# Performance work log

Hardware: AMD Instinct MI355X
Metric: run time of the kernel (lower is better)

The kernel has to match this reference:

```python
import jax, jax.numpy as jnp
import numpy as np

N = 96            # max_nodes == R (all nodes real)
IN_DIM, HID, ZD = 64, 256, 64
E = 1024
U = N * (N - 1) // 2
NUM_LOGITS = U + N   # 4656
MPM_ITERS = 50
BN_EPS = 1e-5

def _xavier_relu(k, fi, fo):
    # xavier_uniform with gain('relu') = sqrt(2)
    s = (2.0 ** 0.5) * (6.0 / (fi + fo)) ** 0.5
    return jax.random.uniform(k, (fi, fo), jnp.float32, -s, s)

def setup_inputs() -> dict:
    key = jax.random.key(0)
    ks = jax.random.split(key, 12)
    x = jax.random.normal(ks[0], (N, IN_DIM), jnp.float32)
    edge_index = jnp.stack([jax.random.randint(ks[1], (E,), 0, N),
                            jax.random.randint(ks[2], (E,), 0, N)]).astype(jnp.int32)
    a = (jax.random.uniform(ks[3], (N, N)) < 0.06).astype(jnp.float32)
    adj_gt = jnp.maximum(a, a.T) * (1.0 - jnp.eye(N, dtype=jnp.float32))
    return dict(
        x=x, edge_index=edge_index, adj_gt=adj_gt,
        W1=_xavier_relu(ks[4], IN_DIM, HID), b1=jnp.zeros(HID, jnp.float32),
        gamma1=jnp.ones(HID, jnp.float32), beta1=jnp.zeros(HID, jnp.float32),
        W2=_xavier_relu(ks[5], HID, HID), b2=jnp.zeros(HID, jnp.float32),
        gamma2=jnp.ones(HID, jnp.float32), beta2=jnp.zeros(HID, jnp.float32),
        Wmu=_xavier_relu(ks[6], HID, ZD), bmu=jnp.zeros(ZD, jnp.float32),
        Wlv=_xavier_relu(ks[7], HID, ZD), blv=jnp.zeros(ZD, jnp.float32),
        Wd1=_xavier_relu(ks[8], ZD, HID), bd1=jnp.zeros(HID, jnp.float32),
        Wd2=_xavier_relu(ks[9], HID, NUM_LOGITS), bd2=jnp.zeros(NUM_LOGITS, jnp.float32),
        eps=jax.random.normal(ks[10], (ZD,), jnp.float32))

def _bn(h, g, b):
    # BatchNorm1d, training mode: normalize over nodes (axis 0)
    m = h.mean(0)
    v = h.var(0)
    return (h - m) * jax.lax.rsqrt(v + BN_EPS) * g + b

def _forward(x, adj_gt, W1, b1, gamma1, beta1, W2, b2, gamma2, beta2,
             Wmu, bmu, Wlv, blv, Wd1, bd1, Wd2, bd2, eps, edge_index):
    ar = jnp.arange(N)
    eye = jnp.eye(N, dtype=bool)
    A = jnp.zeros((N, N), jnp.float32).at[edge_index[0], edge_index[1]].set(1.0)
    A = jnp.maximum(A, jnp.eye(N, dtype=jnp.float32))  # self loops
    dinv = jax.lax.rsqrt(A.sum(1))
    A_norm = A * dinv[:, None] * dinv[None, :]
    h = jax.nn.relu(_bn(A_norm @ (x @ W1) + b1, gamma1, beta1))
    h = jax.nn.relu(_bn(A_norm @ (h @ W2) + b2, gamma2, beta2))
    # ---- readout, reparam, decode ----
    g_vec = h.sum(0) / N                      # divide by real node count R
    mu = g_vec @ Wmu + bmu
    lv = jnp.clip(g_vec @ Wlv + blv, -4.0, 4.0)
    z = mu + eps * jnp.exp(0.5 * lv)
    vec = jnp.tanh(jax.nn.relu(z @ Wd1 + bd1) @ Wd2 + bd2)  # [NUM_LOGITS]
    # ---- vec_to_adj ----
    iu = jnp.triu_indices(N, 1)
    Ah = jnp.zeros((N, N), jnp.float32).at[iu].set(vec[:U])
    Ah = (Ah + Ah.T).at[ar, ar].set(vec[U:])  # adjacency logits
    # ---- edge similarity tensor S[i,j,a,b] ----
    Agt = adj_gt.at[ar, ar].set(1.0)
    B = jax.nn.sigmoid(Ah).at[ar, ar].set(1.0)
    degA, degB = Agt.sum(1), B.sum(1)
    node_sim = 1.0 / (jnp.abs(degA[:, None] - degB[None, :]) + 1.0)  # [N,N]
    dA, dB = jnp.diag(Agt), jnp.diag(B)
    S = (Agt[:, :, None, None] * dA[:, None, None, None] * dA[None, :, None, None]
         * B[None, None, :, :] * dB[None, None, :, None] * dB[None, None, None, :])
    xor = eye[:, :, None, None] ^ eye[None, None, :, :]
    S = jnp.where(xor, 0.0, S)
    diag_val = dA[:, None] * dB[None, :] * node_sim  # value at (i,i,a,a)
    both = eye[:, :, None, None] & eye[None, None, :, :]
    S = jnp.where(both, diag_val[:, None, :, None], S)
    # ---- MPM iteration (fixed 50 steps) ----
    nd = S[ar[:, None], ar[:, None], ar[None, :], ar[None, :]]  # node sim [N,N]
    offmask = (~eye)[:, :, None].astype(S.dtype)                # [N,N,1] over (i,j)
    def step(X, _):
        node_term = X * nd
        XS_max = (S * X[None, :, None, :]).max(-1)  # (i,j,a): max_b X[j,b]*S[i,j,a,b]
        edge_term = (XS_max * offmask).sum(1)       # sum over j != i
        Xn = node_term + edge_term
        Xn = Xn / jnp.linalg.norm(Xn)               # Frobenius norm
        return Xn, None
    X0 = jnp.full((N, N), 1.0 / N, jnp.float32)
    X, _ = jax.lax.scan(jax.checkpoint(step), X0, None, length=MPM_ITERS)
    return X

def reference(x, edge_index, adj_gt, W1, b1, gamma1, beta1, W2, b2, gamma2, beta2,
              Wmu, bmu, Wlv, blv, Wd1, bd1, Wd2, bd2, eps):
    return _forward(x, adj_gt, W1, b1, gamma1, beta1, W2, b2, gamma2, beta2,
                    Wmu, bmu, Wlv, blv, Wd1, bd1, Wd2, bd2, eps, edge_index)
```

## Files before the change

### kernel.cpp

```cpp
#include <hip/hip_runtime.h>
#include <math.h>

#define NN    96
#define EE    1024
#define HID   256
#define IND   64
#define ZD    64
#define NL    4656
#define NBLK  96
#define NTHR  384
#define ITERS 50
#define NBARS 57
#define SHF   (HID*49)

struct Params {
  const float* x; const int* ei; const float* adj;
  const float* W1; const float* b1; const float* g1; const float* be1;
  const float* W2; const float* b2; const float* g2; const float* be2;
  const float* Wmu; const float* bmu; const float* Wlv; const float* blv;
  const float* Wd1; const float* bd1; const float* Wd2; const float* bd2;
  const float* eps; float* out;
};

__device__ float d_XW[NN*HID];
__device__ float d_H1pre[NN*HID];
__device__ float d_HW2[NN*HID];
__device__ float d_H2pre[NN*HID];
__device__ float d_mean1[HID], d_istd1[HID];
__device__ float d_gvec[HID];
__device__ float d_vec[NL];
__device__ float d_Xg[2][NN*NN];
__device__ float d_part[2][NN];
__device__ int   d_flag[NBLK];
__device__ int   d_rel;
__device__ int   d_epoch;

__device__ __forceinline__ float gld(const float* p) {
  return __hip_atomic_load(p, __ATOMIC_RELAXED, __HIP_MEMORY_SCOPE_AGENT);
}
__device__ __forceinline__ void gst(float* p, float v) {
  __hip_atomic_store(p, v, __ATOMIC_RELAXED, __HIP_MEMORY_SCOPE_AGENT);
}

__device__ __forceinline__ float wsum(float v) {
  v += __shfl_xor(v, 32, 64);
  v += __shfl_xor(v, 16, 64);
  v += __shfl_xor(v,  8, 64);
  v += __shfl_xor(v,  4, 64);
  v += __shfl_xor(v,  2, 64);
  v += __shfl_xor(v,  1, 64);
  return v;
}

__device__ __forceinline__ int tri_idx(int a, int c) {
  return a*95 - (a*(a-1))/2 + (c - a - 1);
}

__device__ __forceinline__ void gbar(int idx, int base) {
  asm volatile("s_waitcnt vmcnt(0)" ::: "memory");
  __syncthreads();
  const int tgt = base + idx + 1;
  const int t = threadIdx.x;
  if (blockIdx.x == 0) {
    if (t >= 1 && t < NBLK) {
      while (__hip_atomic_load(&d_flag[t], __ATOMIC_RELAXED, __HIP_MEMORY_SCOPE_AGENT) < tgt)
        __builtin_amdgcn_s_sleep(1);
    }
    __syncthreads();
    if (t == 0)
      __hip_atomic_store(&d_rel, tgt, __ATOMIC_RELAXED, __HIP_MEMORY_SCOPE_AGENT);
  } else {
    if (t == 0) {
      __hip_atomic_store(&d_flag[blockIdx.x], tgt, __ATOMIC_RELAXED, __HIP_MEMORY_SCOPE_AGENT);
      while (__hip_atomic_load(&d_rel, __ATOMIC_RELAXED, __HIP_MEMORY_SCOPE_AGENT) < tgt)
        __builtin_amdgcn_s_sleep(1);
    }
    __syncthreads();
  }
}

__global__ void __launch_bounds__(NTHR) gvae_kernel(Params p) {
  const int b = blockIdx.x;
  const int t = threadIdx.x;

  __shared__ __align__(16) float SH[SHF];
  __shared__ float pre1[HID];
  __shared__ float sg[HID], sd1[HID], sz[ZD];
  __shared__ float dinv[NN];
  __shared__ float eV[NN];   __shared__ int eL[NN];  __shared__ int s_ecnt;
  __shared__ float ndrow[NN], rowsq[NN], xb2[NN];
  __shared__ int   nbrL[NN];
  __shared__ float sdegA;    __shared__ int s_cnt;
  __shared__ float sF;

  const int base = __hip_atomic_load(&d_epoch, __ATOMIC_RELAXED, __HIP_MEMORY_SCOPE_AGENT) * NBARS;

  for (int i = t; i < NN*97; i += NTHR) SH[i] = 0.0f;
  __syncthreads();
  for (int e = t; e < EE; e += NTHR) {
    int s = p.ei[e], d = p.ei[EE + e];
    SH[s*97 + d] = 1.0f;
  }
  if (t < NN) SH[t*97 + t] = 1.0f;
  __syncthreads();
  if (t < NN) {
    float s = 0.0f;
    for (int j = 0; j < NN; ++j) s += SH[t*97 + j];
    dinv[t] = 1.0f / sqrtf(s);
  }
  if (t < 64) {
    bool is1 = SH[b*97 + t] > 0.5f;
    unsigned long long m1 = __ballot(is1);
    if (is1) eL[__popcll(m1 & ((1ull << t) - 1))] = t;
    int c1 = __popcll(m1);
    bool is2 = (t < 32) && SH[b*97 + 64 + t] > 0.5f;
    unsigned long long m2 = __ballot(is2);
    if (is2) eL[c1 + __popcll(m2 & ((1ull << t) - 1))] = 64 + t;
    if (t == 0) s_ecnt = c1 + __popcll(m2);
  }
  __syncthreads();
  if (t < s_ecnt) eV[t] = dinv[b] * dinv[eL[t]];
  if (t < HID) {
    float acc = 0.0f;
    for (int d = 0; d < IND; ++d) acc += p.x[b*IND + d] * p.W1[d*HID + t];
    gst(&d_XW[b*HID + t], acc);
  }
  if (t < NN) gst(&d_Xg[0][b*NN + t], 1.0f/96.0f);
  gbar(0, base);

  {
    const int lim = s_ecnt * HID;
    float tv[16];
    #pragma unroll
    for (int r = 0; r < 16; ++r) {
      int idx = t + r*NTHR;
      if (idx < lim) tv[r] = gld(&d_XW[eL[idx >> 8]*HID + (idx & 255)]);
    }
    #pragma unroll
    for (int r = 0; r < 16; ++r) {
      int idx = t + r*NTHR;
      if (idx < lim) SH[idx] = tv[r];
    }
    for (int idx = t + 16*NTHR; idx < lim; idx += NTHR)
      SH[idx] = gld(&d_XW[eL[idx >> 8]*HID + (idx & 255)]);
    __syncthreads();
    if (t < HID) {
      float acc = 0.0f;
      const int ec = s_ecnt;
      for (int n = 0; n < ec; ++n) acc += eV[n] * SH[n*HID + t];
      acc += p.b1[t];
      pre1[t] = acc;
      gst(&d_H1pre[b*HID + t], acc);
    }
  }
  gbar(1, base);

  if (b < 86) {
    int w = t >> 6, lane = t & 63;
    int c = b*3 + w;
    if (w < 3 && c < HID) {
      float v0 = gld(&d_H1pre[lane*HID + c]);
      float v1 = (lane < 32) ? gld(&d_H1pre[(64+lane)*HID + c]) : 0.0f;
      float mean = wsum(v0 + v1) * (1.0f/96.0f);
      float a0 = v0 - mean, a1 = (lane < 32) ? (v1 - mean) : 0.0f;
      float var = wsum(a0*a0 + a1*a1) * (1.0f/96.0f);
      if (lane == 0) { gst(&d_mean1[c], mean); gst(&d_istd1[c], 1.0f/sqrtf(var + 1e-5f)); }
    }
  }
  gbar(2, base);

  if (t < HID) {
    float m = gld(&d_mean1[t]), is = gld(&d_istd1[t]);
    pre1[t] = fmaxf((pre1[t] - m) * is * p.g1[t] + p.be1[t], 0.0f);
  }
  __syncthreads();
  if (t < HID) {
    float acc = 0.0f;
    for (int k = 0; k < HID; ++k) acc += pre1[k] * p.W2[k*HID + t];
    gst(&d_HW2[b*HID + t], acc);
  }
  gbar(3, base);

  {
    const int lim = s_ecnt * HID;
    float tv[16];
    #pragma unroll
    for (int r = 0; r < 16; ++r) {
      int idx = t + r*NTHR;
      if (idx < lim) tv[r] = gld(&d_HW2[eL[idx >> 8]*HID + (idx & 255)]);
    }
    #pragma unroll
    for (int r = 0; r < 16; ++r) {
      int idx = t + r*NTHR;
      if (idx < lim) SH[idx] = tv[r];
    }
    for (int idx = t + 16*NTHR; idx < lim; idx += NTHR)
      SH[idx] = gld(&d_HW2[eL[idx >> 8]*HID + (idx & 255)]);
    __syncthreads();
    if (t < HID) {
      float acc = 0.0f;
      const int ec = s_ecnt;
      for (int n = 0; n < ec; ++n) acc += eV[n] * SH[n*HID + t];
      acc += p.b2[t];
      gst(&d_H2pre[b*HID + t], acc);
    }
  }
  gbar(4, base);

  if (b < 86) {
    int w = t >> 6, lane = t & 63;
    int c = b*3 + w;
    if (w < 3 && c < HID) {
      float v0 = gld(&d_H2pre[lane*HID + c]);
      float v1 = (lane < 32) ? gld(&d_H2pre[(64+lane)*HID + c]) : 0.0f;
      float mean = wsum(v0 + v1) * (1.0f/96.0f);
      float a0 = v0 - mean, a1 = (lane < 32) ? (v1 - mean) : 0.0f;
      float var = wsum(a0*a0 + a1*a1) * (1.0f/96.0f);
      float is = 1.0f / sqrtf(var + 1e-5f);
      float ga = p.g2[c], be = p.be2[c];
      float h0 = fmaxf((v0 - mean)*is*ga + be, 0.0f);
      float h1v = (lane < 32) ? fmaxf((v1 - mean)*is*ga + be, 0.0f) : 0.0f;
      float gs = wsum(h0 + h1v);
      if (lane == 0) gst(&d_gvec[c], gs * (1.0f/96.0f));
    }
  }
  gbar(5, base);

  if (t < HID) sg[t] = gld(&d_gvec[t]);
  __syncthreads();
  if (t < ZD) {
    float am = p.bmu[t], al = p.blv[t];
    for (int c = 0; c < HID; ++c) {
      float gv = sg[c];
      am += gv * p.Wmu[c*ZD + t];
      al += gv * p.Wlv[c*ZD + t];
    }
    al = fminf(fmaxf(al, -4.0f), 4.0f);
    sz[t] = am + p.eps[t] * expf(0.5f * al);
  }
  __syncthreads();
  if (t < HID) {
    float acc = p.bd1[t];
    for (int d = 0; d < ZD; ++d) acc += sz[d] * p.Wd1[d*HID + t];
    sd1[t] = fmaxf(acc, 0.0f);
  }
  __syncthreads();
  {
    const int o0 = b*49;
    const int nout = min(49, NL - o0);
    #pragma unroll 4
    for (int idx = t; idx < HID*49; idx += NTHR) {
      int k = idx / 49, o = idx - k*49;
      SH[idx] = (o0 + o < NL) ? p.Wd2[k*NL + o0 + o] : 0.0f;
    }
    __syncthreads();
    if (t < nout) {
      float acc = p.bd2[o0 + t];
      for (int k = 0; k < HID; ++k) acc += sd1[k] * SH[k*49 + t];
      gst(&d_vec[o0 + t], tanhf(acc));
    }
  }
  gbar(6, base);

  {
    float tv[13];
    #pragma unroll
    for (int r = 0; r < 13; ++r) {
      int idx = t + r*NTHR;
      if (idx < NL) tv[r] = gld(&d_vec[idx]);
    }
    #pragma unroll
    for (int r = 0; r < 13; ++r) {
      int idx = t + r*NTHR;
      if (idx < NL) SH[idx] = tv[r];
    }
  }
  const int kk = t >> 2;
  const int qq = t & 3;
  if (t < 64) {
    float s = p.adj[b*NN + t] + ((t < 32) ? p.adj[b*NN + 64 + t] : 0.0f);
    s = wsum(s);
    if (t == 0) sdegA = s + 1.0f;
    bool is1 = (t != b) && (p.adj[b*NN + t] > 0.5f);
    unsigned long long m1 = __ballot(is1);
    if (is1) nbrL[__popcll(m1 & ((1ull << t) - 1))] = t;
    int c1 = __popcll(m1);
    bool is2 = (t < 32) && ((64 + t) != b) && (p.adj[b*NN + 64 + t] > 0.5f);
    unsigned long long m2 = __ballot(is2);
    if (is2) nbrL[c1 + __popcll(m2 & ((1ull << t) - 1))] = 64 + t;
    if (t == 0) s_cnt = c1 + __popcll(m2);
  }
  __syncthreads();

  float breg[24];
  {
    float bs = 0.0f;
    const int lb = qq*24;
    #pragma unroll
    for (int s = 0; s < 24; ++s) {
      int l = lb + s;
      float v = 0.0f;
      if (l != kk) {
        int a  = kk < l ? kk : l;
        int cc = kk < l ? l : kk;
        v = 1.0f / (1.0f + expf(-SH[tri_idx(a, cc)]));
      }
      breg[s] = v;
      bs += v;
    }
    float tot = bs + __shfl_xor(bs, 1, 64);
    tot += __shfl_xor(tot, 2, 64);
    if (qq == 0) ndrow[kk] = 1.0f / (fabsf(sdegA - (tot + 1.0f)) + 1.0f);
  }
  __syncthreads();

  int cur = 0;
  for (int it = 0; it < ITERS; ++it) {
    const int cnt = s_cnt;
    const int lim = (cnt + 1) * NN;
    const float* Xs = d_Xg[cur];
    float pj = 0.0f;
    if (it > 0 && t < NN) pj = gld(&d_part[(it-1) & 1][t]);
    float tv[8];
    #pragma unroll
    for (int r = 0; r < 8; ++r) {
      int idx = t + r*NTHR;
      if (idx < lim) {
        int slot = idx / NN, col = idx - slot*NN;
        int j = (slot == cnt) ? b : nbrL[slot];
        tv[r] = gld(&Xs[j*NN + col]);
      }
    }
    float s2 = 1.0f;
    if (it > 0) {
      if (t < NN) rowsq[t] = pj;
      __syncthreads();
      if (t < 64) {
        float v = rowsq[t] + ((t < 32) ? rowsq[64 + t] : 0.0f);
        v = wsum(v);
        if (t == 0) sF = v;
      }
      __syncthreads();
      s2 = sF;
    }
    int ex;
    (void)frexpf(sqrtf(s2), &ex);
    const float scale = ldexpf(1.0f, -ex);
    #pragma unroll
    for (int r = 0; r < 8; ++r) {
      int idx = t + r*NTHR;
      if (idx < lim) SH[idx] = tv[r];
    }
    for (int idx = t + 8*NTHR; idx < lim; idx += NTHR) {
      int slot = idx / NN, col = idx - slot*NN;
      int j = (slot == cnt) ? b : nbrL[slot];
      SH[idx] = gld(&Xs[j*NN + col]);
    }
    __syncthreads();

    float acc = 0.0f;
    for (int n = 0; n < cnt; ++n) {
      const float4* xp = reinterpret_cast<const float4*>(&SH[n*NN + qq*24]);
      float vm = 0.0f;
      #pragma unroll
      for (int s6 = 0; s6 < 6; ++s6) {
        float4 xv = xp[s6];
        vm = fmaxf(vm, breg[4*s6+0] * xv.x);
        vm = fmaxf(vm, breg[4*s6+1] * xv.y);
        vm = fmaxf(vm, breg[4*s6+2] * xv.z);
        vm = fmaxf(vm, breg[4*s6+3] * xv.w);
      }
      vm = fmaxf(vm, __shfl_xor(vm, 1, 64));
      vm = fmaxf(vm, __shfl_xor(vm, 2, 64));
      acc += vm;
    }
    if (qq == 0) {
      float xn = scale * (SH[cnt*NN + kk] * ndrow[kk] + acc);
      xb2[kk] = xn;
      rowsq[kk] = xn * xn;
      gst(&d_Xg[cur ^ 1][b*NN + kk], xn);
    }
    __syncthreads();
    if (t < 64) {
      float v = rowsq[t] + ((t < 32) ? rowsq[64 + t] : 0.0f);
      v = wsum(v);
      if (t == 0) gst(&d_part[it & 1][b], v);
    }
    gbar(7 + it, base);
    cur ^= 1;
  }

  if (t < NN) rowsq[t] = gld(&d_part[(ITERS-1) & 1][t]);
  __syncthreads();
  if (t < 64) {
    float v = rowsq[t] + ((t < 32) ? rowsq[64 + t] : 0.0f);
    v = wsum(v);
    if (t == 0) sF = v;
  }
  __syncthreads();
  if (t < NN) p.out[b*NN + t] = xb2[t] * (1.0f / sqrtf(sF));

  if (b == 0 && t == 0)
    __hip_atomic_fetch_add(&d_epoch, 1, __ATOMIC_RELAXED, __HIP_MEMORY_SCOPE_AGENT);
}

extern "C" void kernel_launch(void* const* d_in, const int* in_sizes, int n_in,
                              void* d_out, int out_size, void* d_ws, size_t ws_size,
                              hipStream_t stream) {
  Params prm;
  prm.x   = (const float*)d_in[0];
  prm.ei  = (const int*  )d_in[1];
  prm.adj = (const float*)d_in[2];
  prm.W1  = (const float*)d_in[3];
  prm.b1  = (const float*)d_in[4];
  prm.g1  = (const float*)d_in[5];
  prm.be1 = (const float*)d_in[6];
  prm.W2  = (const float*)d_in[7];
  prm.b2  = (const float*)d_in[8];
  prm.g2  = (const float*)d_in[9];
  prm.be2 = (const float*)d_in[10];
  prm.Wmu = (const float*)d_in[11];
  prm.bmu = (const float*)d_in[12];
  prm.Wlv = (const float*)d_in[13];
  prm.blv = (const float*)d_in[14];
  prm.Wd1 = (const float*)d_in[15];
  prm.bd1 = (const float*)d_in[16];
  prm.Wd2 = (const float*)d_in[17];
  prm.bd2 = (const float*)d_in[18];
  prm.eps = (const float*)d_in[19];
  prm.out = (float*)d_out;

  void* args[] = { &prm };
  hipLaunchCooperativeKernel(reinterpret_cast<void*>(&gvae_kernel),
                             dim3(NBLK), dim3(NTHR), args, 0, stream);
}
```

Before: 535.6 us.

## Replace per-iteration grid barriers with neighbor-only flags and deferred normalization

The MPM loop no longer applies a global Frobenius normalization each iteration. Each block rescales its own row by a power of two taken from the row max, tracks the accumulated exponent, and publishes data plus an epoch-tagged progress flag. Consumers wait only on their graph neighbors' flags and rebase their values by the exponent difference. Exact normalization happens once at the end with a single grid barrier, which removes 50 global barriers and the per-iteration norm reduction. The risks are floating-point differences from the per-row scaling and a switch from a cooperative launch to a plain one that relies on all blocks being co-resident.

```diff
diff --git a/kernel.cpp b/kernel.cpp
--- a/kernel.cpp
+++ b/kernel.cpp
@@ -10,8 +10,10 @@
 #define NBLK  96
 #define NTHR  384
 #define ITERS 50
-#define NBARS 57
+#define NBARS 8
 #define SHF   (HID*49)
+
+typedef unsigned long long ull;
 
 struct Params {
   const float* x; const int* ei; const float* adj;
@@ -29,8 +31,9 @@
 __device__ float d_mean1[HID], d_istd1[HID];
 __device__ float d_gvec[HID];
 __device__ float d_vec[NL];
-__device__ float d_Xg[2][NN*NN];
-__device__ float d_part[2][NN];
+__device__ float d_P[2][NN*NN];
+__device__ ull   d_prog[2][NN];
+__device__ float d_rssq[NN];
 __device__ int   d_flag[NBLK];
 __device__ int   d_rel;
 __device__ int   d_epoch;
@@ -39,6 +42,12 @@
   return __hip_atomic_load(p, __ATOMIC_RELAXED, __HIP_MEMORY_SCOPE_AGENT);
 }
 __device__ __forceinline__ void gst(float* p, float v) {
+  __hip_atomic_store(p, v, __ATOMIC_RELAXED, __HIP_MEMORY_SCOPE_AGENT);
+}
+__device__ __forceinline__ ull ldp(const ull* p) {
+  return __hip_atomic_load(p, __ATOMIC_RELAXED, __HIP_MEMORY_SCOPE_AGENT);
+}
+__device__ __forceinline__ void stp(ull* p, ull v) {
   __hip_atomic_store(p, v, __ATOMIC_RELAXED, __HIP_MEMORY_SCOPE_AGENT);
 }
 
@@ -51,6 +60,15 @@
   v += __shfl_xor(v,  1, 64);
   return v;
 }
+__device__ __forceinline__ float wmax(float v) {
+  v = fmaxf(v, __shfl_xor(v, 32, 64));
+  v = fmaxf(v, __shfl_xor(v, 16, 64));
+  v = fmaxf(v, __shfl_xor(v,  8, 64));
+  v = fmaxf(v, __shfl_xor(v,  4, 64));
+  v = fmaxf(v, __shfl_xor(v,  2, 64));
+  v = fmaxf(v, __shfl_xor(v,  1, 64));
+  return v;
+}
 
 __device__ __forceinline__ int tri_idx(int a, int c) {
   return a*95 - (a*(a-1))/2 + (c - a - 1);
@@ -90,10 +108,13 @@
   __shared__ float eV[NN];   __shared__ int eL[NN];  __shared__ int s_ecnt;
   __shared__ float ndrow[NN], rowsq[NN], xb2[NN];
   __shared__ int   nbrL[NN];
+  __shared__ int   s_dE[NN];
   __shared__ float sdegA;    __shared__ int s_cnt;
-  __shared__ float sF;
-
-  const int base = __hip_atomic_load(&d_epoch, __ATOMIC_RELAXED, __HIP_MEMORY_SCOPE_AGENT) * NBARS;
+  __shared__ float sF;       __shared__ int s_ei;  __shared__ int s_emax;
+
+  const int epoch = __hip_atomic_load(&d_epoch, __ATOMIC_RELAXED, __HIP_MEMORY_SCOPE_AGENT);
+  const int base  = epoch * NBARS;
+  const ull ep64  = (ull)epoch * 64ull;
 
   for (int i = t; i < NN*97; i += NTHR) SH[i] = 0.0f;
   __syncthreads();
@@ -110,11 +131,11 @@
   }
   if (t < 64) {
     bool is1 = SH[b*97 + t] > 0.5f;
-    unsigned long long m1 = __ballot(is1);
+    ull m1 = __ballot(is1);
     if (is1) eL[__popcll(m1 & ((1ull << t) - 1))] = t;
     int c1 = __popcll(m1);
     bool is2 = (t < 32) && SH[b*97 + 64 + t] > 0.5f;
-    unsigned long long m2 = __ballot(is2);
+    ull m2 = __ballot(is2);
     if (is2) eL[c1 + __popcll(m2 & ((1ull << t) - 1))] = 64 + t;
     if (t == 0) s_ecnt = c1 + __popcll(m2);
   }
@@ -125,7 +146,6 @@
     for (int d = 0; d < IND; ++d) acc += p.x[b*IND + d] * p.W1[d*HID + t];
     gst(&d_XW[b*HID + t], acc);
   }
-  if (t < NN) gst(&d_Xg[0][b*NN + t], 1.0f/96.0f);
   gbar(0, base);
 
   {
@@ -282,11 +302,11 @@
     s = wsum(s);
     if (t == 0) sdegA = s + 1.0f;
     bool is1 = (t != b) && (p.adj[b*NN + t] > 0.5f);
-    unsigned long long m1 = __ballot(is1);
+    ull m1 = __ballot(is1);
     if (is1) nbrL[__popcll(m1 & ((1ull << t) - 1))] = t;
     int c1 = __popcll(m1);
     bool is2 = (t < 32) && ((64 + t) != b) && (p.adj[b*NN + 64 + t] > 0.5f);
-    unsigned long long m2 = __ballot(is2);
+    ull m2 = __ballot(is2);
     if (is2) nbrL[c1 + __popcll(m2 & ((1ull << t) - 1))] = 64 + t;
     if (t == 0) s_cnt = c1 + __popcll(m2);
   }
@@ -314,50 +334,71 @@
   }
   __syncthreads();
 
-  int cur = 0;
-  for (int it = 0; it < ITERS; ++it) {
-    const int cnt = s_cnt;
-    const int lim = (cnt + 1) * NN;
-    const float* Xs = d_Xg[cur];
-    float pj = 0.0f;
-    if (it > 0 && t < NN) pj = gld(&d_part[(it-1) & 1][t]);
-    float tv[8];
-    #pragma unroll
-    for (int r = 0; r < 8; ++r) {
-      int idx = t + r*NTHR;
-      if (idx < lim) {
+  const int cnt = s_cnt;
+  int E_own = 0;
+
+  {
+    float vm = 0.0f;
+    #pragma unroll
+    for (int s = 0; s < 24; ++s) vm = fmaxf(vm, breg[s] * (1.0f/96.0f));
+    vm = fmaxf(vm, __shfl_xor(vm, 1, 64));
+    vm = fmaxf(vm, __shfl_xor(vm, 2, 64));
+    float acc = 0.0f;
+    for (int n = 0; n < cnt; ++n) acc += vm;
+    if (qq == 0) xb2[kk] = (1.0f/96.0f) * ndrow[kk] + acc;
+  }
+  __syncthreads();
+  if (t < 64) {
+    float m = xb2[t];
+    if (t < 32) m = fmaxf(m, xb2[64 + t]);
+    m = wmax(m);
+    if (t == 0) s_ei = ilogbf(m);
+  }
+  __syncthreads();
+  E_own += s_ei;
+  if (qq == 0) {
+    float Pv = ldexpf(xb2[kk], -s_ei);
+    xb2[kk] = Pv;
+    gst(&d_P[1][b*NN + kk], Pv);
+  }
+  asm volatile("s_waitcnt vmcnt(0)" ::: "memory");
+  __syncthreads();
+  if (t == 0) stp(&d_prog[1][b], ((ep64 + 1ull) << 16) | (ull)(E_own & 0xFFFF));
+
+  for (int it = 2; it <= ITERS; ++it) {
+    const int pb = (it - 1) & 1;
+    if (t < cnt) {
+      const int j = nbrL[t];
+      const ull want = ep64 + (ull)(it - 1);
+      ull f;
+      while (((f = ldp(&d_prog[pb][j])) >> 16) < want)
+        __builtin_amdgcn_s_sleep(1);
+      s_dE[t] = (int)(short)(f & 0xFFFF) - E_own;
+    }
+    __syncthreads();
+    const int lim = cnt * NN;
+    {
+      float tv[8]; int te[8];
+      #pragma unroll
+      for (int r = 0; r < 8; ++r) {
+        int idx = t + r*NTHR;
+        if (idx < lim) {
+          int slot = idx / NN, col = idx - slot*NN;
+          tv[r] = gld(&d_P[pb][nbrL[slot]*NN + col]);
+          te[r] = s_dE[slot];
+        }
+      }
+      #pragma unroll
+      for (int r = 0; r < 8; ++r) {
+        int idx = t + r*NTHR;
+        if (idx < lim) SH[idx] = ldexpf(tv[r], te[r]);
+      }
+      for (int idx = t + 8*NTHR; idx < lim; idx += NTHR) {
         int slot = idx / NN, col = idx - slot*NN;
-        int j = (slot == cnt) ? b : nbrL[slot];
-        tv[r] = gld(&Xs[j*NN + col]);
+        SH[idx] = ldexpf(gld(&d_P[pb][nbrL[slot]*NN + col]), s_dE[slot]);
       }
     }
-    float s2 = 1.0f;
-    if (it > 0) {
-      if (t < NN) rowsq[t] = pj;
-      __syncthreads();
-      if (t < 64) {
-        float v = rowsq[t] + ((t < 32) ? rowsq[64 + t] : 0.0f);
-        v = wsum(v);
-        if (t == 0) sF = v;
-      }
-      __syncthreads();
-      s2 = sF;
-    }
-    int ex;
-    (void)frexpf(sqrtf(s2), &ex);
-    const float scale = ldexpf(1.0f, -ex);
-    #pragma unroll
-    for (int r = 0; r < 8; ++r) {
-      int idx = t + r*NTHR;
-      if (idx < lim) SH[idx] = tv[r];
-    }
-    for (int idx = t + 8*NTHR; idx < lim; idx += NTHR) {
-      int slot = idx / NN, col = idx - slot*NN;
-      int j = (slot == cnt) ? b : nbrL[slot];
-      SH[idx] = gld(&Xs[j*NN + col]);
-    }
-    __syncthreads();
-
+    __syncthreads();
     float acc = 0.0f;
     for (int n = 0; n < cnt; ++n) {
       const float4* xp = reinterpret_cast<const float4*>(&SH[n*NN + qq*24]);
@@ -374,31 +415,50 @@
       vm = fmaxf(vm, __shfl_xor(vm, 2, 64));
       acc += vm;
     }
+    if (qq == 0) xb2[kk] = xb2[kk] * ndrow[kk] + acc;
+    __syncthreads();
+    if (t < 64) {
+      float m = xb2[t];
+      if (t < 32) m = fmaxf(m, xb2[64 + t]);
+      m = wmax(m);
+      if (t == 0) s_ei = ilogbf(m);
+    }
+    __syncthreads();
+    E_own += s_ei;
     if (qq == 0) {
-      float xn = scale * (SH[cnt*NN + kk] * ndrow[kk] + acc);
-      xb2[kk] = xn;
-      rowsq[kk] = xn * xn;
-      gst(&d_Xg[cur ^ 1][b*NN + kk], xn);
-    }
-    __syncthreads();
-    if (t < 64) {
-      float v = rowsq[t] + ((t < 32) ? rowsq[64 + t] : 0.0f);
-      v = wsum(v);
-      if (t == 0) gst(&d_part[it & 1][b], v);
-    }
-    gbar(7 + it, base);
-    cur ^= 1;
-  }
-
-  if (t < NN) rowsq[t] = gld(&d_part[(ITERS-1) & 1][t]);
+      float Pv = ldexpf(xb2[kk], -s_ei);
+      xb2[kk] = Pv;
+      gst(&d_P[it & 1][b*NN + kk], Pv);
+    }
+    asm volatile("s_waitcnt vmcnt(0)" ::: "memory");
+    __syncthreads();
+    if (t == 0) stp(&d_prog[it & 1][b], ((ep64 + (ull)it) << 16) | (ull)(E_own & 0xFFFF));
+  }
+
+  if (t < NN) rowsq[t] = xb2[t] * xb2[t];
   __syncthreads();
   if (t < 64) {
     float v = rowsq[t] + ((t < 32) ? rowsq[64 + t] : 0.0f);
     v = wsum(v);
-    if (t == 0) sF = v;
-  }
-  __syncthreads();
-  if (t < NN) p.out[b*NN + t] = xb2[t] * (1.0f / sqrtf(sF));
+    if (t == 0) gst(&d_rssq[b], v);
+  }
+  gbar(7, base);
+  if (t < NN) {
+    ull f = ldp(&d_prog[ITERS & 1][t]);
+    s_dE[t] = (int)(short)(f & 0xFFFF);
+    rowsq[t] = gld(&d_rssq[t]);
+  }
+  __syncthreads();
+  if (t == 0) {
+    int em = s_dE[0];
+    for (int j = 1; j < NN; ++j) em = max(em, s_dE[j]);
+    float s = 0.0f;
+    for (int j = 0; j < NN; ++j) s += ldexpf(rowsq[j], 2*(s_dE[j] - em));
+    s_emax = em;
+    sF = 1.0f / sqrtf(s);
+  }
+  __syncthreads();
+  if (t < NN) p.out[b*NN + t] = ldexpf(xb2[t] * sF, E_own - s_emax);
 
   if (b == 0 && t == 0)
     __hip_atomic_fetch_add(&d_epoch, 1, __ATOMIC_RELAXED, __HIP_MEMORY_SCOPE_AGENT);
@@ -430,7 +490,5 @@
   prm.eps = (const float*)d_in[19];
   prm.out = (float*)d_out;
 
-  void* args[] = { &prm };
-  hipLaunchCooperativeKernel(reinterpret_cast<void*>(&gvae_kernel),
-                             dim3(NBLK), dim3(NTHR), args, 0, stream);
-}
+  gvae_kernel<<<dim3(NBLK), dim3(NTHR), 0, stream>>>(prm);
+}
```

Measured after the change: 459.1 us. -14.3%, faster.
